# Kernel tuning notes

Hardware: AMD Instinct MI355X
Metric: run time of the kernel (lower is better)

Reference implementation:

```python
import jax, jax.numpy as jnp
import numpy as np

B, S, E, A, DK, H = 8, 2048, 256, 16, 64, 64  # batch, seq, embed, action, d_key, mlp hidden


def setup_inputs() -> dict:
    key = jax.random.key(0)
    ks = jax.random.split(key, 8)
    obs = jax.random.normal(ks[0], (B, S, E), dtype=jnp.float32)
    act = jnp.zeros((B, S, A), dtype=jnp.float32)  # one-hot actions; unused by forward
    # projection weights stored as [in, out] (torch Linear applies x @ W.T)
    Wq = jax.random.normal(ks[1], (E, DK), dtype=jnp.float32) / np.sqrt(E)
    Wk = jax.random.normal(ks[2], (E, DK), dtype=jnp.float32) / np.sqrt(E)
    Wv = jax.random.normal(ks[3], (E, DK), dtype=jnp.float32) / np.sqrt(E)
    W1 = jax.random.normal(ks[4], (DK, H), dtype=jnp.float32) / np.sqrt(DK)
    b1 = jnp.zeros((H,), dtype=jnp.float32)
    W2 = jax.random.normal(ks[5], (H, 1), dtype=jnp.float32) / np.sqrt(H)
    b2 = jnp.zeros((1,), dtype=jnp.float32)
    return dict(obs=obs, act=act, Wq=Wq, Wk=Wk, Wv=Wv, W1=W1, b1=b1, W2=W2, b2=b2)


def reference(obs, act, Wq, Wk, Wv, W1, b1, W2, b2):
    b, s, _ = obs.shape
    dk = Wq.shape[1]
    scale = dk ** -0.25  # applied to both q and k, net 1/sqrt(dk)
    q = (obs @ Wq) * scale          # [b, s, dk]
    k = (obs @ Wk) * scale          # [b, s, dk]
    v = obs @ Wv                    # [b, s, dk]
    scores = jnp.einsum('bqd,bkd->bqk', q, k)  # [b, s, s]
    causal = jnp.tril(jnp.ones((s, s), dtype=bool))
    scores = jnp.where(causal[None], scores, -jnp.inf)
    attn = jax.nn.softmax(scores, axis=2)      # [b, s, s]
    attn_out = jnp.einsum('bqk,bkd->bqd', attn, v)  # [b, s, dk]
    h = jax.nn.relu(attn_out.reshape(b * s, dk) @ W1 + b1)
    x = h @ W2 + b2                 # [b*s, 1]
    return (x, attn)
```

## Files before the change

### kernel.cpp

```cpp
#include <hip/hip_runtime.h>
#include <hip/hip_bf16.h>
#include <math.h>

#define NB 8
#define SQ 2048
#define EMB 256

typedef __attribute__((ext_vector_type(8))) short short8;
typedef __attribute__((ext_vector_type(4))) float f32x4;

__device__ __forceinline__ short f2bf(float f) {
    union { float f; unsigned u; } v; v.f = f;
    unsigned r = v.u + 0x7FFF + ((v.u >> 16) & 1);
    return (short)(r >> 16);
}

__global__ __launch_bounds__(256) void k_wt(const float* __restrict__ Wq,
                                            const float* __restrict__ Wk,
                                            const float* __restrict__ Wv,
                                            short* __restrict__ wt) {
    int o = blockIdx.x * 256 + threadIdx.x;
    int row = o >> 8, e = o & 255;
    int w = row >> 6, d = row & 63;
    const float* W = (w == 0) ? Wq : ((w == 1) ? Wk : Wv);
    wt[o] = f2bf(W[e * 64 + d]);
}

__global__ __launch_bounds__(256) void k_proj(const float* __restrict__ obs,
                                              const short* __restrict__ wt,
                                              short* __restrict__ qw,
                                              short* __restrict__ kw,
                                              short* __restrict__ vt) {
    int tid = threadIdx.x, w = tid >> 6, l = tid & 63;
    int rb = blockIdx.x;
    int r0 = rb * 64 + w * 16;
    int arow = r0 + (l & 15);
    int eo = (l >> 4) * 8;
    f32x4 acc[12];
    #pragma unroll
    for (int c = 0; c < 12; ++c) acc[c] = (f32x4){0.f, 0.f, 0.f, 0.f};
    #pragma unroll
    for (int ks = 0; ks < 8; ++ks) {
        int e0 = ks * 32;
        const float* ap = obs + (size_t)arow * 256 + e0 + eo;
        float4 f0 = *(const float4*)ap;
        float4 f1 = *(const float4*)(ap + 4);
        short8 a;
        a[0] = f2bf(f0.x); a[1] = f2bf(f0.y); a[2] = f2bf(f0.z); a[3] = f2bf(f0.w);
        a[4] = f2bf(f1.x); a[5] = f2bf(f1.y); a[6] = f2bf(f1.z); a[7] = f2bf(f1.w);
        #pragma unroll
        for (int c = 0; c < 12; ++c) {
            short8 bf = *(const short8*)(wt + (size_t)(c * 16 + (l & 15)) * 256 + e0 + eo);
            acc[c] = __builtin_amdgcn_mfma_f32_16x16x32_bf16(a, bf, acc[c], 0, 0, 0);
        }
    }
    const float scale = 0.35355339059327373f;
    __shared__ short ldsv[64][72];
    int rloc = w * 16 + (l >> 4) * 4;
    int col16 = l & 15;
    #pragma unroll
    for (int c = 0; c < 12; ++c) {
        #pragma unroll
        for (int r = 0; r < 4; ++r) {
            float val = acc[c][r];
            int row = r0 + (l >> 4) * 4 + r;
            if (c < 4) {
                qw[(size_t)row * 64 + c * 16 + col16] = f2bf(val * scale);
            } else if (c < 8) {
                kw[(size_t)row * 64 + (c - 4) * 16 + col16] = f2bf(val * scale);
            } else {
                ldsv[(c - 8) * 16 + col16][rloc + r] = f2bf(val);
            }
        }
    }
    __syncthreads();
    int b = (rb * 64) >> 11;
    int s0 = (rb * 64) & 2047;
    int d = tid >> 2, ch = (tid & 3) * 16;
    short* dst = vt + (size_t)b * 64 * 2048 + (size_t)d * 2048 + s0 + ch;
    #pragma unroll
    for (int j = 0; j < 16; ++j) dst[j] = ldsv[d][ch + j];
}

__global__ __launch_bounds__(256) void k_flash(const short* __restrict__ qw,
                                               const short* __restrict__ kw,
                                               const short* __restrict__ vt,
                                               float* __restrict__ ao,
                                               float* __restrict__ ml) {
    int qb = blockIdx.x, b = blockIdx.y;
    int q0 = qb * 64;
    int tid = threadIdx.x, w = tid >> 6, l = tid & 63;
    int lg = l >> 4, lc = l & 15;
    int r0 = q0 + w * 16;
    int eo = lg * 8;
    __shared__ short ldsP[4][16][72];
    const short* qbase = qw + (size_t)b * SQ * 64;
    const short* kbase = kw + (size_t)b * SQ * 64;
    const short* vbase = vt + (size_t)b * 64 * SQ;
    short8 qf0 = *(const short8*)(qbase + (size_t)(r0 + lc) * 64 + eo);
    short8 qf1 = *(const short8*)(qbase + (size_t)(r0 + lc) * 64 + 32 + eo);
    float m[4], lsum[4];
    f32x4 o[4];
    #pragma unroll
    for (int r = 0; r < 4; ++r) { m[r] = -INFINITY; lsum[r] = 0.f; }
    #pragma unroll
    for (int nj = 0; nj < 4; ++nj) o[nj] = (f32x4){0.f, 0.f, 0.f, 0.f};

    for (int kb = 0; kb <= qb; ++kb) {
        int k0 = kb * 64;
        f32x4 s[4];
        #pragma unroll
        for (int nj = 0; nj < 4; ++nj) s[nj] = (f32x4){0.f, 0.f, 0.f, 0.f};
        #pragma unroll
        for (int nj = 0; nj < 4; ++nj) {
            short8 kf = *(const short8*)(kbase + (size_t)(k0 + nj * 16 + lc) * 64 + eo);
            s[nj] = __builtin_amdgcn_mfma_f32_16x16x32_bf16(qf0, kf, s[nj], 0, 0, 0);
        }
        #pragma unroll
        for (int nj = 0; nj < 4; ++nj) {
            short8 kf = *(const short8*)(kbase + (size_t)(k0 + nj * 16 + lc) * 64 + 32 + eo);
            s[nj] = __builtin_amdgcn_mfma_f32_16x16x32_bf16(qf1, kf, s[nj], 0, 0, 0);
        }
        if (kb == qb) {
            #pragma unroll
            for (int nj = 0; nj < 4; ++nj)
                #pragma unroll
                for (int r = 0; r < 4; ++r)
                    if (k0 + nj * 16 + lc > r0 + lg * 4 + r) s[nj][r] = -INFINITY;
        }
        #pragma unroll
        for (int r = 0; r < 4; ++r) {
            float pm = fmaxf(fmaxf(s[0][r], s[1][r]), fmaxf(s[2][r], s[3][r]));
            pm = fmaxf(pm, __shfl_xor(pm, 1));
            pm = fmaxf(pm, __shfl_xor(pm, 2));
            pm = fmaxf(pm, __shfl_xor(pm, 4));
            pm = fmaxf(pm, __shfl_xor(pm, 8));
            float mn = fmaxf(m[r], pm);
            float sc = __expf(m[r] - mn);
            m[r] = mn;
            lsum[r] *= sc;
            #pragma unroll
            for (int nj = 0; nj < 4; ++nj) o[nj][r] *= sc;
            float ps = 0.f;
            #pragma unroll
            for (int nj = 0; nj < 4; ++nj) {
                float p = __expf(s[nj][r] - mn);
                ps += p;
                ldsP[w][lg * 4 + r][nj * 16 + lc] = f2bf(p);
            }
            ps += __shfl_xor(ps, 1);
            ps += __shfl_xor(ps, 2);
            ps += __shfl_xor(ps, 4);
            ps += __shfl_xor(ps, 8);
            lsum[r] += ps;
        }
        #pragma unroll
        for (int ks = 0; ks < 2; ++ks) {
            short8 pa = *(const short8*)&ldsP[w][lc][ks * 32 + lg * 8];
            #pragma unroll
            for (int nj = 0; nj < 4; ++nj) {
                short8 vf = *(const short8*)(vbase + (size_t)(nj * 16 + lc) * SQ + k0 + ks * 32 + eo);
                o[nj] = __builtin_amdgcn_mfma_f32_16x16x32_bf16(pa, vf, o[nj], 0, 0, 0);
            }
        }
    }
    #pragma unroll
    for (int r = 0; r < 4; ++r) {
        float inv = 1.f / lsum[r];
        int row = r0 + lg * 4 + r;
        if (lc == 0) {
            ml[((size_t)b * SQ + row) * 2]     = m[r];
            ml[((size_t)b * SQ + row) * 2 + 1] = inv;
        }
        #pragma unroll
        for (int nj = 0; nj < 4; ++nj)
            ao[((size_t)b * SQ + row) * 64 + nj * 16 + lc] = o[nj][r] * inv;
    }
}

__global__ __launch_bounds__(256) void k_attnw(const short* __restrict__ qw,
                                               const short* __restrict__ kw,
                                               const float* __restrict__ ml,
                                               float* __restrict__ attn) {
    int kb = blockIdx.x, qb = blockIdx.y, b = blockIdx.z;
    int q0 = qb * 64, k0 = kb * 64;
    float* abase = attn + (size_t)b * SQ * SQ;
    int tid = threadIdx.x;
    if (kb > qb) {
        int row = q0 + (tid >> 2);
        float4* dst = (float4*)(abase + (size_t)row * SQ + k0 + (tid & 3) * 16);
        float4 z = {0.f, 0.f, 0.f, 0.f};
        dst[0] = z; dst[1] = z; dst[2] = z; dst[3] = z;
        return;
    }
    int w = tid >> 6, l = tid & 63, lg = l >> 4, lc = l & 15;
    int r0 = q0 + w * 16, eo = lg * 8;
    const short* qbase = qw + (size_t)b * SQ * 64;
    const short* kbase = kw + (size_t)b * SQ * 64;
    short8 qf0 = *(const short8*)(qbase + (size_t)(r0 + lc) * 64 + eo);
    short8 qf1 = *(const short8*)(qbase + (size_t)(r0 + lc) * 64 + 32 + eo);
    f32x4 s[4];
    #pragma unroll
    for (int nj = 0; nj < 4; ++nj) s[nj] = (f32x4){0.f, 0.f, 0.f, 0.f};
    #pragma unroll
    for (int nj = 0; nj < 4; ++nj) {
        short8 kf = *(const short8*)(kbase + (size_t)(k0 + nj * 16 + lc) * 64 + eo);
        s[nj] = __builtin_amdgcn_mfma_f32_16x16x32_bf16(qf0, kf, s[nj], 0, 0, 0);
    }
    #pragma unroll
    for (int nj = 0; nj < 4; ++nj) {
        short8 kf = *(const short8*)(kbase + (size_t)(k0 + nj * 16 + lc) * 64 + 32 + eo);
        s[nj] = __builtin_amdgcn_mfma_f32_16x16x32_bf16(qf1, kf, s[nj], 0, 0, 0);
    }
    #pragma unroll
    for (int r = 0; r < 4; ++r) {
        int row = r0 + lg * 4 + r;
        float mr = ml[((size_t)b * SQ + row) * 2];
        float iv = ml[((size_t)b * SQ + row) * 2 + 1];
        #pragma unroll
        for (int nj = 0; nj < 4; ++nj) {
            int col = k0 + nj * 16 + lc;
            float p = (col <= row) ? __expf(s[nj][r] - mr) * iv : 0.f;
            abase[(size_t)row * SQ + col] = p;
        }
    }
}

__global__ __launch_bounds__(256) void k_mlp(const float* __restrict__ ao,
                                             const float* __restrict__ W1,
                                             const float* __restrict__ b1,
                                             const float* __restrict__ W2,
                                             const float* __restrict__ b2,
                                             float* __restrict__ x) {
    int tid = threadIdx.x, w = tid >> 6, l = tid & 63;
    int grow = blockIdx.x * 4 + w;
    __shared__ float lds[4][64];
    lds[w][l] = ao[(size_t)grow * 64 + l];
    __syncthreads();
    float acc = b1[l];
    #pragma unroll
    for (int d = 0; d < 64; ++d) acc += lds[w][d] * W1[d * 64 + l];
    float h = fmaxf(acc, 0.f);
    float p = h * W2[l];
    #pragma unroll
    for (int o = 32; o > 0; o >>= 1) p += __shfl_xor(p, o);
    if (l == 0) x[grow] = p + b2[0];
}

extern "C" void kernel_launch(void* const* d_in, const int* in_sizes, int n_in,
                              void* d_out, int out_size, void* d_ws, size_t ws_size,
                              hipStream_t stream) {
    const float* obs = (const float*)d_in[0];
    const float* Wq  = (const float*)d_in[2];
    const float* Wk  = (const float*)d_in[3];
    const float* Wv  = (const float*)d_in[4];
    const float* W1  = (const float*)d_in[5];
    const float* b1  = (const float*)d_in[6];
    const float* W2  = (const float*)d_in[7];
    const float* b2  = (const float*)d_in[8];

    float* x    = (float*)d_out;
    float* attn = (float*)d_out + NB * SQ;

    char* ws = (char*)d_ws;
    short* wt = (short*)(ws);
    short* qw = (short*)(ws + 131072);
    short* kw = (short*)(ws + 2228224);
    short* vt = (short*)(ws + 4325376);
    float* ml = (float*)(ws + 6422528);
    float* ao = (float*)(ws + 6553600);

    k_wt<<<dim3(192), dim3(256), 0, stream>>>(Wq, Wk, Wv, wt);
    k_proj<<<dim3(256), dim3(256), 0, stream>>>(obs, wt, qw, kw, vt);
    k_flash<<<dim3(32, NB), dim3(256), 0, stream>>>(qw, kw, vt, ao, ml);
    k_attnw<<<dim3(32, 32, NB), dim3(256), 0, stream>>>(qw, kw, ml, attn);
    k_mlp<<<dim3(4096), dim3(256), 0, stream>>>(ao, W1, b1, W2, b2, x);
}
```

Measured before the change: 152.4 us.

## Fuse flash attention, attention-weight write and MLP into one split-K kernel

Merges the flash-attention, attention-matrix and MLP kernels into a single kernel. Each 512-thread block handles 32 query rows and splits the key blocks across 8 waves, then merges the partial softmax states through LDS atomics. Blocks are scheduled heaviest-first, and the intermediate attention output and max/sum buffers no longer make a round trip through global memory. The projection kernel is also re-tiled to 16 rows per block for more parallelism. The cost is that QK^T is computed twice within one kernel, plus extra LDS reduction and barriers.

```diff
diff --git a/kernel.cpp b/kernel.cpp
--- a/kernel.cpp
+++ b/kernel.cpp
@@ -4,7 +4,8 @@
 
 #define NB 8
 #define SQ 2048
-#define EMB 256
+#define QR 32
+#define NW 8
 
 typedef __attribute__((ext_vector_type(8))) short short8;
 typedef __attribute__((ext_vector_type(4))) float f32x4;
@@ -26,225 +27,250 @@
     wt[o] = f2bf(W[e * 64 + d]);
 }
 
-__global__ __launch_bounds__(256) void k_proj(const float* __restrict__ obs,
-                                              const short* __restrict__ wt,
-                                              short* __restrict__ qw,
-                                              short* __restrict__ kw,
-                                              short* __restrict__ vt) {
-    int tid = threadIdx.x, w = tid >> 6, l = tid & 63;
-    int rb = blockIdx.x;
-    int r0 = rb * 64 + w * 16;
-    int arow = r0 + (l & 15);
-    int eo = (l >> 4) * 8;
-    f32x4 acc[12];
-    #pragma unroll
-    for (int c = 0; c < 12; ++c) acc[c] = (f32x4){0.f, 0.f, 0.f, 0.f};
+__global__ __launch_bounds__(256, 4) void k_proj(const float* __restrict__ obs,
+                                                 const short* __restrict__ wt,
+                                                 short* __restrict__ qw,
+                                                 short* __restrict__ kw,
+                                                 short* __restrict__ vt) {
+    int tid = threadIdx.x, w = tid >> 6, l = tid & 63, lg = l >> 4, lc = l & 15;
+    int r0 = blockIdx.x * 16;
+    int arow = r0 + lc;
+    f32x4 accq = {0.f,0.f,0.f,0.f}, acck = {0.f,0.f,0.f,0.f}, accv = {0.f,0.f,0.f,0.f};
+    const short* wq = wt + (size_t)(w * 16 + lc) * 256;
+    const short* wk = wt + (size_t)(64 + w * 16 + lc) * 256;
+    const short* wv = wt + (size_t)(128 + w * 16 + lc) * 256;
     #pragma unroll
     for (int ks = 0; ks < 8; ++ks) {
-        int e0 = ks * 32;
-        const float* ap = obs + (size_t)arow * 256 + e0 + eo;
+        int e0 = ks * 32 + lg * 8;
+        const float* ap = obs + (size_t)arow * 256 + e0;
         float4 f0 = *(const float4*)ap;
         float4 f1 = *(const float4*)(ap + 4);
         short8 a;
         a[0] = f2bf(f0.x); a[1] = f2bf(f0.y); a[2] = f2bf(f0.z); a[3] = f2bf(f0.w);
         a[4] = f2bf(f1.x); a[5] = f2bf(f1.y); a[6] = f2bf(f1.z); a[7] = f2bf(f1.w);
-        #pragma unroll
-        for (int c = 0; c < 12; ++c) {
-            short8 bf = *(const short8*)(wt + (size_t)(c * 16 + (l & 15)) * 256 + e0 + eo);
-            acc[c] = __builtin_amdgcn_mfma_f32_16x16x32_bf16(a, bf, acc[c], 0, 0, 0);
-        }
+        accq = __builtin_amdgcn_mfma_f32_16x16x32_bf16(a, *(const short8*)(wq + e0), accq, 0, 0, 0);
+        acck = __builtin_amdgcn_mfma_f32_16x16x32_bf16(a, *(const short8*)(wk + e0), acck, 0, 0, 0);
+        accv = __builtin_amdgcn_mfma_f32_16x16x32_bf16(a, *(const short8*)(wv + e0), accv, 0, 0, 0);
     }
     const float scale = 0.35355339059327373f;
-    __shared__ short ldsv[64][72];
-    int rloc = w * 16 + (l >> 4) * 4;
-    int col16 = l & 15;
-    #pragma unroll
-    for (int c = 0; c < 12; ++c) {
-        #pragma unroll
-        for (int r = 0; r < 4; ++r) {
-            float val = acc[c][r];
-            int row = r0 + (l >> 4) * 4 + r;
-            if (c < 4) {
-                qw[(size_t)row * 64 + c * 16 + col16] = f2bf(val * scale);
-            } else if (c < 8) {
-                kw[(size_t)row * 64 + (c - 4) * 16 + col16] = f2bf(val * scale);
-            } else {
-                ldsv[(c - 8) * 16 + col16][rloc + r] = f2bf(val);
-            }
-        }
+    __shared__ short ldsv[64][18];
+    #pragma unroll
+    for (int r = 0; r < 4; ++r) {
+        int row = r0 + lg * 4 + r;
+        qw[(size_t)row * 64 + w * 16 + lc] = f2bf(accq[r] * scale);
+        kw[(size_t)row * 64 + w * 16 + lc] = f2bf(acck[r] * scale);
+        ldsv[w * 16 + lc][lg * 4 + r] = f2bf(accv[r]);
     }
     __syncthreads();
-    int b = (rb * 64) >> 11;
-    int s0 = (rb * 64) & 2047;
-    int d = tid >> 2, ch = (tid & 3) * 16;
-    short* dst = vt + (size_t)b * 64 * 2048 + (size_t)d * 2048 + s0 + ch;
-    #pragma unroll
-    for (int j = 0; j < 16; ++j) dst[j] = ldsv[d][ch + j];
-}
-
-__global__ __launch_bounds__(256) void k_flash(const short* __restrict__ qw,
-                                               const short* __restrict__ kw,
-                                               const short* __restrict__ vt,
-                                               float* __restrict__ ao,
-                                               float* __restrict__ ml) {
-    int qb = blockIdx.x, b = blockIdx.y;
-    int q0 = qb * 64;
-    int tid = threadIdx.x, w = tid >> 6, l = tid & 63;
-    int lg = l >> 4, lc = l & 15;
-    int r0 = q0 + w * 16;
-    int eo = lg * 8;
-    __shared__ short ldsP[4][16][72];
+    int b = r0 >> 11, s0 = r0 & 2047;
+    int d = tid >> 2, sc = (tid & 3) * 4;
+    short* dst = vt + (size_t)b * 64 * SQ + (size_t)d * SQ + s0 + sc;
+    dst[0] = ldsv[d][sc]; dst[1] = ldsv[d][sc + 1];
+    dst[2] = ldsv[d][sc + 2]; dst[3] = ldsv[d][sc + 3];
+}
+
+__global__ __launch_bounds__(512, 2) void k_fused(const short* __restrict__ qw,
+                                                  const short* __restrict__ kw,
+                                                  const short* __restrict__ vt,
+                                                  const float* __restrict__ W1,
+                                                  const float* __restrict__ b1,
+                                                  const float* __restrict__ W2,
+                                                  const float* __restrict__ b2,
+                                                  float* __restrict__ x,
+                                                  float* __restrict__ attn) {
+    int bx = blockIdx.x;
+    int sq = 63 - (bx >> 3);
+    int b  = bx & 7;
+    int s0 = sq * QR;
+    int tid = threadIdx.x, w = tid >> 6, l = tid & 63, lg = l >> 4, lc = l & 15;
+    int kbmax = sq >> 1;
+
+    __shared__ short ldsP[NW][QR][72];
+    __shared__ float o_acc[QR][72];
+    __shared__ float mw[NW][QR], lw[NW][QR];
+    __shared__ float mfin[QR], linv[QR];
+
     const short* qbase = qw + (size_t)b * SQ * 64;
     const short* kbase = kw + (size_t)b * SQ * 64;
     const short* vbase = vt + (size_t)b * 64 * SQ;
-    short8 qf0 = *(const short8*)(qbase + (size_t)(r0 + lc) * 64 + eo);
-    short8 qf1 = *(const short8*)(qbase + (size_t)(r0 + lc) * 64 + 32 + eo);
-    float m[4], lsum[4];
-    f32x4 o[4];
-    #pragma unroll
-    for (int r = 0; r < 4; ++r) { m[r] = -INFINITY; lsum[r] = 0.f; }
-    #pragma unroll
-    for (int nj = 0; nj < 4; ++nj) o[nj] = (f32x4){0.f, 0.f, 0.f, 0.f};
-
-    for (int kb = 0; kb <= qb; ++kb) {
+
+    short8 qf[2][2];
+    #pragma unroll
+    for (int mi = 0; mi < 2; ++mi)
+        #pragma unroll
+        for (int ks = 0; ks < 2; ++ks)
+            qf[mi][ks] = *(const short8*)(qbase + (size_t)(s0 + mi * 16 + lc) * 64 + ks * 32 + lg * 8);
+
+    f32x4 o[2][4];
+    float m[8], ls[8];
+    #pragma unroll
+    for (int i = 0; i < 8; ++i) { m[i] = -INFINITY; ls[i] = 0.f; }
+    #pragma unroll
+    for (int mi = 0; mi < 2; ++mi)
+        #pragma unroll
+        for (int nj = 0; nj < 4; ++nj) o[mi][nj] = (f32x4){0.f,0.f,0.f,0.f};
+
+    for (int kb = w; kb <= kbmax; kb += NW) {
         int k0 = kb * 64;
-        f32x4 s[4];
-        #pragma unroll
-        for (int nj = 0; nj < 4; ++nj) s[nj] = (f32x4){0.f, 0.f, 0.f, 0.f};
+        f32x4 s[2][4];
+        #pragma unroll
+        for (int mi = 0; mi < 2; ++mi)
+            #pragma unroll
+            for (int nj = 0; nj < 4; ++nj) s[mi][nj] = (f32x4){0.f,0.f,0.f,0.f};
         #pragma unroll
         for (int nj = 0; nj < 4; ++nj) {
-            short8 kf = *(const short8*)(kbase + (size_t)(k0 + nj * 16 + lc) * 64 + eo);
-            s[nj] = __builtin_amdgcn_mfma_f32_16x16x32_bf16(qf0, kf, s[nj], 0, 0, 0);
-        }
+            short8 kf0 = *(const short8*)(kbase + (size_t)(k0 + nj * 16 + lc) * 64 + lg * 8);
+            short8 kf1 = *(const short8*)(kbase + (size_t)(k0 + nj * 16 + lc) * 64 + 32 + lg * 8);
+            #pragma unroll
+            for (int mi = 0; mi < 2; ++mi) {
+                s[mi][nj] = __builtin_amdgcn_mfma_f32_16x16x32_bf16(qf[mi][0], kf0, s[mi][nj], 0, 0, 0);
+                s[mi][nj] = __builtin_amdgcn_mfma_f32_16x16x32_bf16(qf[mi][1], kf1, s[mi][nj], 0, 0, 0);
+            }
+        }
+        if (kb == kbmax) {
+            #pragma unroll
+            for (int mi = 0; mi < 2; ++mi)
+                #pragma unroll
+                for (int nj = 0; nj < 4; ++nj)
+                    #pragma unroll
+                    for (int r = 0; r < 4; ++r)
+                        if (k0 + nj * 16 + lc > s0 + mi * 16 + lg * 4 + r) s[mi][nj][r] = -INFINITY;
+        }
+        #pragma unroll
+        for (int mi = 0; mi < 2; ++mi)
+            #pragma unroll
+            for (int r = 0; r < 4; ++r) {
+                int ri = mi * 4 + r;
+                int rowloc = mi * 16 + lg * 4 + r;
+                float pm = fmaxf(fmaxf(s[mi][0][r], s[mi][1][r]), fmaxf(s[mi][2][r], s[mi][3][r]));
+                pm = fmaxf(pm, __shfl_xor(pm, 1));
+                pm = fmaxf(pm, __shfl_xor(pm, 2));
+                pm = fmaxf(pm, __shfl_xor(pm, 4));
+                pm = fmaxf(pm, __shfl_xor(pm, 8));
+                float mn = fmaxf(m[ri], pm);
+                float sc = __expf(m[ri] - mn);
+                m[ri] = mn;
+                ls[ri] *= sc;
+                #pragma unroll
+                for (int nj = 0; nj < 4; ++nj) o[mi][nj][r] *= sc;
+                float ps = 0.f;
+                #pragma unroll
+                for (int nj = 0; nj < 4; ++nj) {
+                    float p = __expf(s[mi][nj][r] - mn);
+                    ps += p;
+                    ldsP[w][rowloc][nj * 16 + lc] = f2bf(p);
+                }
+                ps += __shfl_xor(ps, 1);
+                ps += __shfl_xor(ps, 2);
+                ps += __shfl_xor(ps, 4);
+                ps += __shfl_xor(ps, 8);
+                ls[ri] += ps;
+            }
+        #pragma unroll
+        for (int ks = 0; ks < 2; ++ks) {
+            short8 pa0 = *(const short8*)&ldsP[w][lc][ks * 32 + lg * 8];
+            short8 pa1 = *(const short8*)&ldsP[w][16 + lc][ks * 32 + lg * 8];
+            #pragma unroll
+            for (int nj = 0; nj < 4; ++nj) {
+                short8 vf = *(const short8*)(vbase + (size_t)(nj * 16 + lc) * SQ + k0 + ks * 32 + lg * 8);
+                o[0][nj] = __builtin_amdgcn_mfma_f32_16x16x32_bf16(pa0, vf, o[0][nj], 0, 0, 0);
+                o[1][nj] = __builtin_amdgcn_mfma_f32_16x16x32_bf16(pa1, vf, o[1][nj], 0, 0, 0);
+            }
+        }
+    }
+
+    #pragma unroll
+    for (int mi = 0; mi < 2; ++mi)
+        #pragma unroll
+        for (int r = 0; r < 4; ++r) {
+            int rowloc = mi * 16 + lg * 4 + r;
+            if (lc == 0) { mw[w][rowloc] = m[mi * 4 + r]; lw[w][rowloc] = ls[mi * 4 + r]; }
+        }
+    for (int idx = tid; idx < QR * 72; idx += 512) ((float*)o_acc)[idx] = 0.f;
+    __syncthreads();
+    #pragma unroll
+    for (int mi = 0; mi < 2; ++mi)
+        #pragma unroll
+        for (int r = 0; r < 4; ++r) {
+            int rowloc = mi * 16 + lg * 4 + r;
+            float mf = mw[0][rowloc];
+            #pragma unroll
+            for (int ww = 1; ww < NW; ++ww) mf = fmaxf(mf, mw[ww][rowloc]);
+            float f = __expf(m[mi * 4 + r] - mf);
+            #pragma unroll
+            for (int nj = 0; nj < 4; ++nj)
+                atomicAdd(&o_acc[rowloc][nj * 16 + lc], o[mi][nj][r] * f);
+        }
+    __syncthreads();
+
+    #pragma unroll
+    for (int rr = 0; rr < 4; ++rr) {
+        int rowloc = w * 4 + rr;
+        float mf = mw[0][rowloc];
+        #pragma unroll
+        for (int ww = 1; ww < NW; ++ww) mf = fmaxf(mf, mw[ww][rowloc]);
+        float lf = 0.f;
+        #pragma unroll
+        for (int ww = 0; ww < NW; ++ww) lf += __expf(mw[ww][rowloc] - mf) * lw[ww][rowloc];
+        float inv = 1.f / lf;
+        if (l == 0) { mfin[rowloc] = mf; linv[rowloc] = inv; }
+        float t = 0.f;
+        #pragma unroll 8
+        for (int d = 0; d < 64; ++d) t += o_acc[rowloc][d] * W1[d * 64 + l];
+        float h = fmaxf(t * inv + b1[l], 0.f);
+        float px = h * W2[l];
+        px += __shfl_xor(px, 1);
+        px += __shfl_xor(px, 2);
+        px += __shfl_xor(px, 4);
+        px += __shfl_xor(px, 8);
+        px += __shfl_xor(px, 16);
+        px += __shfl_xor(px, 32);
+        if (l == 0) x[(size_t)b * SQ + s0 + rowloc] = px + b2[0];
+    }
+    __syncthreads();
+
+    float* abase = attn + (size_t)b * SQ * SQ;
+    for (int kb = w; kb < 32; kb += NW) {
+        int k0 = kb * 64;
+        if (kb > kbmax) {
+            float4 z = {0.f,0.f,0.f,0.f};
+            #pragma unroll
+            for (int rep = 0; rep < 8; ++rep) {
+                int row = s0 + rep * 4 + lg;
+                *(float4*)(abase + (size_t)row * SQ + k0 + lc * 4) = z;
+            }
+            continue;
+        }
+        f32x4 s[2][4];
+        #pragma unroll
+        for (int mi = 0; mi < 2; ++mi)
+            #pragma unroll
+            for (int nj = 0; nj < 4; ++nj) s[mi][nj] = (f32x4){0.f,0.f,0.f,0.f};
         #pragma unroll
         for (int nj = 0; nj < 4; ++nj) {
-            short8 kf = *(const short8*)(kbase + (size_t)(k0 + nj * 16 + lc) * 64 + 32 + eo);
-            s[nj] = __builtin_amdgcn_mfma_f32_16x16x32_bf16(qf1, kf, s[nj], 0, 0, 0);
-        }
-        if (kb == qb) {
-            #pragma unroll
-            for (int nj = 0; nj < 4; ++nj)
+            short8 kf0 = *(const short8*)(kbase + (size_t)(k0 + nj * 16 + lc) * 64 + lg * 8);
+            short8 kf1 = *(const short8*)(kbase + (size_t)(k0 + nj * 16 + lc) * 64 + 32 + lg * 8);
+            #pragma unroll
+            for (int mi = 0; mi < 2; ++mi) {
+                s[mi][nj] = __builtin_amdgcn_mfma_f32_16x16x32_bf16(qf[mi][0], kf0, s[mi][nj], 0, 0, 0);
+                s[mi][nj] = __builtin_amdgcn_mfma_f32_16x16x32_bf16(qf[mi][1], kf1, s[mi][nj], 0, 0, 0);
+            }
+        }
+        #pragma unroll
+        for (int mi = 0; mi < 2; ++mi)
+            #pragma unroll
+            for (int r = 0; r < 4; ++r) {
+                int rowloc = mi * 16 + lg * 4 + r;
+                int row = s0 + rowloc;
+                float mf = mfin[rowloc], iv = linv[rowloc];
                 #pragma unroll
-                for (int r = 0; r < 4; ++r)
-                    if (k0 + nj * 16 + lc > r0 + lg * 4 + r) s[nj][r] = -INFINITY;
-        }
-        #pragma unroll
-        for (int r = 0; r < 4; ++r) {
-            float pm = fmaxf(fmaxf(s[0][r], s[1][r]), fmaxf(s[2][r], s[3][r]));
-            pm = fmaxf(pm, __shfl_xor(pm, 1));
-            pm = fmaxf(pm, __shfl_xor(pm, 2));
-            pm = fmaxf(pm, __shfl_xor(pm, 4));
-            pm = fmaxf(pm, __shfl_xor(pm, 8));
-            float mn = fmaxf(m[r], pm);
-            float sc = __expf(m[r] - mn);
-            m[r] = mn;
-            lsum[r] *= sc;
-            #pragma unroll
-            for (int nj = 0; nj < 4; ++nj) o[nj][r] *= sc;
-            float ps = 0.f;
-            #pragma unroll
-            for (int nj = 0; nj < 4; ++nj) {
-                float p = __expf(s[nj][r] - mn);
-                ps += p;
-                ldsP[w][lg * 4 + r][nj * 16 + lc] = f2bf(p);
-            }
-            ps += __shfl_xor(ps, 1);
-            ps += __shfl_xor(ps, 2);
-            ps += __shfl_xor(ps, 4);
-            ps += __shfl_xor(ps, 8);
-            lsum[r] += ps;
-        }
-        #pragma unroll
-        for (int ks = 0; ks < 2; ++ks) {
-            short8 pa = *(const short8*)&ldsP[w][lc][ks * 32 + lg * 8];
-            #pragma unroll
-            for (int nj = 0; nj < 4; ++nj) {
-                short8 vf = *(const short8*)(vbase + (size_t)(nj * 16 + lc) * SQ + k0 + ks * 32 + eo);
-                o[nj] = __builtin_amdgcn_mfma_f32_16x16x32_bf16(pa, vf, o[nj], 0, 0, 0);
-            }
-        }
-    }
-    #pragma unroll
-    for (int r = 0; r < 4; ++r) {
-        float inv = 1.f / lsum[r];
-        int row = r0 + lg * 4 + r;
-        if (lc == 0) {
-            ml[((size_t)b * SQ + row) * 2]     = m[r];
-            ml[((size_t)b * SQ + row) * 2 + 1] = inv;
-        }
-        #pragma unroll
-        for (int nj = 0; nj < 4; ++nj)
-            ao[((size_t)b * SQ + row) * 64 + nj * 16 + lc] = o[nj][r] * inv;
-    }
-}
-
-__global__ __launch_bounds__(256) void k_attnw(const short* __restrict__ qw,
-                                               const short* __restrict__ kw,
-                                               const float* __restrict__ ml,
-                                               float* __restrict__ attn) {
-    int kb = blockIdx.x, qb = blockIdx.y, b = blockIdx.z;
-    int q0 = qb * 64, k0 = kb * 64;
-    float* abase = attn + (size_t)b * SQ * SQ;
-    int tid = threadIdx.x;
-    if (kb > qb) {
-        int row = q0 + (tid >> 2);
-        float4* dst = (float4*)(abase + (size_t)row * SQ + k0 + (tid & 3) * 16);
-        float4 z = {0.f, 0.f, 0.f, 0.f};
-        dst[0] = z; dst[1] = z; dst[2] = z; dst[3] = z;
-        return;
-    }
-    int w = tid >> 6, l = tid & 63, lg = l >> 4, lc = l & 15;
-    int r0 = q0 + w * 16, eo = lg * 8;
-    const short* qbase = qw + (size_t)b * SQ * 64;
-    const short* kbase = kw + (size_t)b * SQ * 64;
-    short8 qf0 = *(const short8*)(qbase + (size_t)(r0 + lc) * 64 + eo);
-    short8 qf1 = *(const short8*)(qbase + (size_t)(r0 + lc) * 64 + 32 + eo);
-    f32x4 s[4];
-    #pragma unroll
-    for (int nj = 0; nj < 4; ++nj) s[nj] = (f32x4){0.f, 0.f, 0.f, 0.f};
-    #pragma unroll
-    for (int nj = 0; nj < 4; ++nj) {
-        short8 kf = *(const short8*)(kbase + (size_t)(k0 + nj * 16 + lc) * 64 + eo);
-        s[nj] = __builtin_amdgcn_mfma_f32_16x16x32_bf16(qf0, kf, s[nj], 0, 0, 0);
-    }
-    #pragma unroll
-    for (int nj = 0; nj < 4; ++nj) {
-        short8 kf = *(const short8*)(kbase + (size_t)(k0 + nj * 16 + lc) * 64 + 32 + eo);
-        s[nj] = __builtin_amdgcn_mfma_f32_16x16x32_bf16(qf1, kf, s[nj], 0, 0, 0);
-    }
-    #pragma unroll
-    for (int r = 0; r < 4; ++r) {
-        int row = r0 + lg * 4 + r;
-        float mr = ml[((size_t)b * SQ + row) * 2];
-        float iv = ml[((size_t)b * SQ + row) * 2 + 1];
-        #pragma unroll
-        for (int nj = 0; nj < 4; ++nj) {
-            int col = k0 + nj * 16 + lc;
-            float p = (col <= row) ? __expf(s[nj][r] - mr) * iv : 0.f;
-            abase[(size_t)row * SQ + col] = p;
-        }
-    }
-}
-
-__global__ __launch_bounds__(256) void k_mlp(const float* __restrict__ ao,
-                                             const float* __restrict__ W1,
-                                             const float* __restrict__ b1,
-                                             const float* __restrict__ W2,
-                                             const float* __restrict__ b2,
-                                             float* __restrict__ x) {
-    int tid = threadIdx.x, w = tid >> 6, l = tid & 63;
-    int grow = blockIdx.x * 4 + w;
-    __shared__ float lds[4][64];
-    lds[w][l] = ao[(size_t)grow * 64 + l];
-    __syncthreads();
-    float acc = b1[l];
-    #pragma unroll
-    for (int d = 0; d < 64; ++d) acc += lds[w][d] * W1[d * 64 + l];
-    float h = fmaxf(acc, 0.f);
-    float p = h * W2[l];
-    #pragma unroll
-    for (int o = 32; o > 0; o >>= 1) p += __shfl_xor(p, o);
-    if (l == 0) x[grow] = p + b2[0];
+                for (int nj = 0; nj < 4; ++nj) {
+                    int col = k0 + nj * 16 + lc;
+                    float p = (col <= row) ? __expf(s[mi][nj][r] - mf) * iv : 0.f;
+                    abase[(size_t)row * SQ + col] = p;
+                }
+            }
+    }
 }
 
 extern "C" void kernel_launch(void* const* d_in, const int* in_sizes, int n_in,
@@ -267,12 +293,8 @@
     short* qw = (short*)(ws + 131072);
     short* kw = (short*)(ws + 2228224);
     short* vt = (short*)(ws + 4325376);
-    float* ml = (float*)(ws + 6422528);
-    float* ao = (float*)(ws + 6553600);
 
     k_wt<<<dim3(192), dim3(256), 0, stream>>>(Wq, Wk, Wv, wt);
-    k_proj<<<dim3(256), dim3(256), 0, stream>>>(obs, wt, qw, kw, vt);
-    k_flash<<<dim3(32, NB), dim3(256), 0, stream>>>(qw, kw, vt, ao, ml);
-    k_attnw<<<dim3(32, 32, NB), dim3(256), 0, stream>>>(qw, kw, ml, attn);
-    k_mlp<<<dim3(4096), dim3(256), 0, stream>>>(ao, W1, b1, W2, b2, x);
-}
+    k_proj<<<dim3(1024), dim3(256), 0, stream>>>(obs, wt, qw, kw, vt);
+    k_fused<<<dim3(512), dim3(512), 0, stream>>>(qw, kw, vt, W1, b1, W2, b2, x, attn);
+}
```

New measurement: 136.9 us. 10.2% less time.

## Split flash attention across key blocks and fuse combine with MLP

Applied to the files above, without the earlier changes.

The flash kernel now splits each query block's key loop across eight strided partitions, which raises the block count from 256 to up to 2048. It writes unnormalized partial outputs and (m, l) pairs into the attn output buffer, which serves as scratch until k_attnw overwrites it. A new combine kernel merges the partitions with log-sum-exp weights, writes the final m and 1/l, and runs the MLP in the same kernel, so the separate MLP launch and the ao round trip are gone. The projection kernel is also regridded to 16 rows per block with 4x more blocks. The combine step adds extra global traffic for the partials, and its scalar MLP loop runs with fewer blocks.

```diff
diff --git a/kernel.cpp b/kernel.cpp
--- a/kernel.cpp
+++ b/kernel.cpp
@@ -4,7 +4,7 @@
 
 #define NB 8
 #define SQ 2048
-#define EMB 256
+#define NSP 8
 
 typedef __attribute__((ext_vector_type(8))) short short8;
 typedef __attribute__((ext_vector_type(4))) float f32x4;
@@ -26,71 +26,57 @@
     wt[o] = f2bf(W[e * 64 + d]);
 }
 
-__global__ __launch_bounds__(256) void k_proj(const float* __restrict__ obs,
-                                              const short* __restrict__ wt,
-                                              short* __restrict__ qw,
-                                              short* __restrict__ kw,
-                                              short* __restrict__ vt) {
-    int tid = threadIdx.x, w = tid >> 6, l = tid & 63;
-    int rb = blockIdx.x;
-    int r0 = rb * 64 + w * 16;
-    int arow = r0 + (l & 15);
-    int eo = (l >> 4) * 8;
-    f32x4 acc[12];
-    #pragma unroll
-    for (int c = 0; c < 12; ++c) acc[c] = (f32x4){0.f, 0.f, 0.f, 0.f};
+__global__ __launch_bounds__(256, 4) void k_proj(const float* __restrict__ obs,
+                                                 const short* __restrict__ wt,
+                                                 short* __restrict__ qw,
+                                                 short* __restrict__ kw,
+                                                 short* __restrict__ vt) {
+    int tid = threadIdx.x, w = tid >> 6, l = tid & 63, lg = l >> 4, lc = l & 15;
+    int r0 = blockIdx.x * 16;
+    int arow = r0 + lc;
+    f32x4 accq = {0.f,0.f,0.f,0.f}, acck = {0.f,0.f,0.f,0.f}, accv = {0.f,0.f,0.f,0.f};
+    const short* wq = wt + (size_t)(w * 16 + lc) * 256;
+    const short* wk = wt + (size_t)(64 + w * 16 + lc) * 256;
+    const short* wv = wt + (size_t)(128 + w * 16 + lc) * 256;
     #pragma unroll
     for (int ks = 0; ks < 8; ++ks) {
-        int e0 = ks * 32;
-        const float* ap = obs + (size_t)arow * 256 + e0 + eo;
+        int e0 = ks * 32 + lg * 8;
+        const float* ap = obs + (size_t)arow * 256 + e0;
         float4 f0 = *(const float4*)ap;
         float4 f1 = *(const float4*)(ap + 4);
         short8 a;
         a[0] = f2bf(f0.x); a[1] = f2bf(f0.y); a[2] = f2bf(f0.z); a[3] = f2bf(f0.w);
         a[4] = f2bf(f1.x); a[5] = f2bf(f1.y); a[6] = f2bf(f1.z); a[7] = f2bf(f1.w);
-        #pragma unroll
-        for (int c = 0; c < 12; ++c) {
-            short8 bf = *(const short8*)(wt + (size_t)(c * 16 + (l & 15)) * 256 + e0 + eo);
-            acc[c] = __builtin_amdgcn_mfma_f32_16x16x32_bf16(a, bf, acc[c], 0, 0, 0);
-        }
+        accq = __builtin_amdgcn_mfma_f32_16x16x32_bf16(a, *(const short8*)(wq + e0), accq, 0, 0, 0);
+        acck = __builtin_amdgcn_mfma_f32_16x16x32_bf16(a, *(const short8*)(wk + e0), acck, 0, 0, 0);
+        accv = __builtin_amdgcn_mfma_f32_16x16x32_bf16(a, *(const short8*)(wv + e0), accv, 0, 0, 0);
     }
     const float scale = 0.35355339059327373f;
-    __shared__ short ldsv[64][72];
-    int rloc = w * 16 + (l >> 4) * 4;
-    int col16 = l & 15;
-    #pragma unroll
-    for (int c = 0; c < 12; ++c) {
-        #pragma unroll
-        for (int r = 0; r < 4; ++r) {
-            float val = acc[c][r];
-            int row = r0 + (l >> 4) * 4 + r;
-            if (c < 4) {
-                qw[(size_t)row * 64 + c * 16 + col16] = f2bf(val * scale);
-            } else if (c < 8) {
-                kw[(size_t)row * 64 + (c - 4) * 16 + col16] = f2bf(val * scale);
-            } else {
-                ldsv[(c - 8) * 16 + col16][rloc + r] = f2bf(val);
-            }
-        }
+    __shared__ short ldsv[64][18];
+    #pragma unroll
+    for (int r = 0; r < 4; ++r) {
+        int row = r0 + lg * 4 + r;
+        qw[(size_t)row * 64 + w * 16 + lc] = f2bf(accq[r] * scale);
+        kw[(size_t)row * 64 + w * 16 + lc] = f2bf(acck[r] * scale);
+        ldsv[w * 16 + lc][lg * 4 + r] = f2bf(accv[r]);
     }
     __syncthreads();
-    int b = (rb * 64) >> 11;
-    int s0 = (rb * 64) & 2047;
-    int d = tid >> 2, ch = (tid & 3) * 16;
-    short* dst = vt + (size_t)b * 64 * 2048 + (size_t)d * 2048 + s0 + ch;
-    #pragma unroll
-    for (int j = 0; j < 16; ++j) dst[j] = ldsv[d][ch + j];
+    int b = r0 >> 11, s0 = r0 & 2047;
+    int d = tid >> 2, sc = (tid & 3) * 4;
+    short* dst = vt + (size_t)b * 64 * SQ + (size_t)d * SQ + s0 + sc;
+    dst[0] = ldsv[d][sc]; dst[1] = ldsv[d][sc + 1];
+    dst[2] = ldsv[d][sc + 2]; dst[3] = ldsv[d][sc + 3];
 }
 
 __global__ __launch_bounds__(256) void k_flash(const short* __restrict__ qw,
                                                const short* __restrict__ kw,
                                                const short* __restrict__ vt,
-                                               float* __restrict__ ao,
-                                               float* __restrict__ ml) {
-    int qb = blockIdx.x, b = blockIdx.y;
+                                               float* __restrict__ op,
+                                               float* __restrict__ mlpart) {
+    int qb = blockIdx.x, sp = blockIdx.y, b = blockIdx.z;
+    if (sp > qb) return;
     int q0 = qb * 64;
-    int tid = threadIdx.x, w = tid >> 6, l = tid & 63;
-    int lg = l >> 4, lc = l & 15;
+    int tid = threadIdx.x, w = tid >> 6, l = tid & 63, lg = l >> 4, lc = l & 15;
     int r0 = q0 + w * 16;
     int eo = lg * 8;
     __shared__ short ldsP[4][16][72];
@@ -106,7 +92,7 @@
     #pragma unroll
     for (int nj = 0; nj < 4; ++nj) o[nj] = (f32x4){0.f, 0.f, 0.f, 0.f};
 
-    for (int kb = 0; kb <= qb; ++kb) {
+    for (int kb = sp; kb <= qb; kb += NSP) {
         int k0 = kb * 64;
         f32x4 s[4];
         #pragma unroll
@@ -164,23 +150,100 @@
             }
         }
     }
+    size_t pb = ((size_t)sp * NB + b) * SQ;
     #pragma unroll
     for (int r = 0; r < 4; ++r) {
-        float inv = 1.f / lsum[r];
         int row = r0 + lg * 4 + r;
         if (lc == 0) {
-            ml[((size_t)b * SQ + row) * 2]     = m[r];
-            ml[((size_t)b * SQ + row) * 2 + 1] = inv;
+            mlpart[(pb + row) * 2]     = m[r];
+            mlpart[(pb + row) * 2 + 1] = lsum[r];
         }
         #pragma unroll
         for (int nj = 0; nj < 4; ++nj)
-            ao[((size_t)b * SQ + row) * 64 + nj * 16 + lc] = o[nj][r] * inv;
+            op[(pb + row) * 64 + nj * 16 + lc] = o[nj][r];
+    }
+}
+
+__global__ __launch_bounds__(256) void k_combine(const float* __restrict__ op,
+                                                 const float* __restrict__ mlpart,
+                                                 const float* __restrict__ W1,
+                                                 const float* __restrict__ b1,
+                                                 const float* __restrict__ W2,
+                                                 const float* __restrict__ b2,
+                                                 float* __restrict__ x,
+                                                 float* __restrict__ mlf) {
+    int qb = blockIdx.x, b = blockIdx.y;
+    int s0 = qb * 64;
+    int nsp = (qb + 1 < NSP) ? (qb + 1) : NSP;
+    int tid = threadIdx.x;
+    __shared__ float wgt[NSP][64];
+    __shared__ float linv_s[64];
+    __shared__ float ao[64][68];
+    if (tid < 64) {
+        int row = s0 + tid;
+        float mm[NSP], ll[NSP];
+        float mf = -INFINITY;
+        #pragma unroll
+        for (int sp = 0; sp < NSP; ++sp) {
+            if (sp < nsp) {
+                mm[sp] = mlpart[(((size_t)sp * NB + b) * SQ + row) * 2];
+                ll[sp] = mlpart[(((size_t)sp * NB + b) * SQ + row) * 2 + 1];
+            } else { mm[sp] = -INFINITY; ll[sp] = 0.f; }
+            mf = fmaxf(mf, mm[sp]);
+        }
+        float lf = 0.f;
+        #pragma unroll
+        for (int sp = 0; sp < NSP; ++sp) {
+            float wv = __expf(mm[sp] - mf);
+            wgt[sp][tid] = wv;
+            lf += wv * ll[sp];
+        }
+        float inv = 1.f / lf;
+        linv_s[tid] = inv;
+        mlf[((size_t)b * SQ + row) * 2]     = mf;
+        mlf[((size_t)b * SQ + row) * 2 + 1] = inv;
+    }
+    __syncthreads();
+    int row = tid >> 2, cg = (tid & 3) * 16;
+    float acc[16];
+    #pragma unroll
+    for (int j = 0; j < 16; ++j) acc[j] = 0.f;
+    for (int sp = 0; sp < NSP; ++sp) {
+        if (sp >= nsp) break;
+        const float* src = op + (((size_t)sp * NB + b) * SQ + s0 + row) * 64 + cg;
+        float wv = wgt[sp][row];
+        #pragma unroll
+        for (int j = 0; j < 4; ++j) {
+            float4 v = *(const float4*)(src + j * 4);
+            acc[j*4+0] += wv * v.x; acc[j*4+1] += wv * v.y;
+            acc[j*4+2] += wv * v.z; acc[j*4+3] += wv * v.w;
+        }
+    }
+    float inv = linv_s[row];
+    #pragma unroll
+    for (int j = 0; j < 16; ++j) ao[row][cg + j] = acc[j] * inv;
+    __syncthreads();
+    int w = tid >> 6, l = tid & 63;
+    for (int rr = 0; rr < 16; ++rr) {
+        int rowloc = w * 16 + rr;
+        float t = 0.f;
+        #pragma unroll 8
+        for (int d = 0; d < 64; ++d) t += ao[rowloc][d] * W1[d * 64 + l];
+        float h = fmaxf(t + b1[l], 0.f);
+        float px = h * W2[l];
+        px += __shfl_xor(px, 1);
+        px += __shfl_xor(px, 2);
+        px += __shfl_xor(px, 4);
+        px += __shfl_xor(px, 8);
+        px += __shfl_xor(px, 16);
+        px += __shfl_xor(px, 32);
+        if (l == 0) x[(size_t)b * SQ + s0 + rowloc] = px + b2[0];
     }
 }
 
 __global__ __launch_bounds__(256) void k_attnw(const short* __restrict__ qw,
                                                const short* __restrict__ kw,
-                                               const float* __restrict__ ml,
+                                               const float* __restrict__ mlf,
                                                float* __restrict__ attn) {
     int kb = blockIdx.x, qb = blockIdx.y, b = blockIdx.z;
     int q0 = qb * 64, k0 = kb * 64;
@@ -215,8 +278,8 @@
     #pragma unroll
     for (int r = 0; r < 4; ++r) {
         int row = r0 + lg * 4 + r;
-        float mr = ml[((size_t)b * SQ + row) * 2];
-        float iv = ml[((size_t)b * SQ + row) * 2 + 1];
+        float mr = mlf[((size_t)b * SQ + row) * 2];
+        float iv = mlf[((size_t)b * SQ + row) * 2 + 1];
         #pragma unroll
         for (int nj = 0; nj < 4; ++nj) {
             int col = k0 + nj * 16 + lc;
@@ -224,27 +287,6 @@
             abase[(size_t)row * SQ + col] = p;
         }
     }
-}
-
-__global__ __launch_bounds__(256) void k_mlp(const float* __restrict__ ao,
-                                             const float* __restrict__ W1,
-                                             const float* __restrict__ b1,
-                                             const float* __restrict__ W2,
-                                             const float* __restrict__ b2,
-                                             float* __restrict__ x) {
-    int tid = threadIdx.x, w = tid >> 6, l = tid & 63;
-    int grow = blockIdx.x * 4 + w;
-    __shared__ float lds[4][64];
-    lds[w][l] = ao[(size_t)grow * 64 + l];
-    __syncthreads();
-    float acc = b1[l];
-    #pragma unroll
-    for (int d = 0; d < 64; ++d) acc += lds[w][d] * W1[d * 64 + l];
-    float h = fmaxf(acc, 0.f);
-    float p = h * W2[l];
-    #pragma unroll
-    for (int o = 32; o > 0; o >>= 1) p += __shfl_xor(p, o);
-    if (l == 0) x[grow] = p + b2[0];
 }
 
 extern "C" void kernel_launch(void* const* d_in, const int* in_sizes, int n_in,
@@ -262,17 +304,19 @@
     float* x    = (float*)d_out;
     float* attn = (float*)d_out + NB * SQ;
 
+    float* op     = attn;
+    float* mlpart = attn + (size_t)NSP * NB * SQ * 64;
+
     char* ws = (char*)d_ws;
-    short* wt = (short*)(ws);
-    short* qw = (short*)(ws + 131072);
-    short* kw = (short*)(ws + 2228224);
-    short* vt = (short*)(ws + 4325376);
-    float* ml = (float*)(ws + 6422528);
-    float* ao = (float*)(ws + 6553600);
+    short* wt  = (short*)(ws);
+    short* qw  = (short*)(ws + 131072);
+    short* kw  = (short*)(ws + 2228224);
+    short* vt  = (short*)(ws + 4325376);
+    float* mlf = (float*)(ws + 6422528);
 
     k_wt<<<dim3(192), dim3(256), 0, stream>>>(Wq, Wk, Wv, wt);
-    k_proj<<<dim3(256), dim3(256), 0, stream>>>(obs, wt, qw, kw, vt);
-    k_flash<<<dim3(32, NB), dim3(256), 0, stream>>>(qw, kw, vt, ao, ml);
-    k_attnw<<<dim3(32, 32, NB), dim3(256), 0, stream>>>(qw, kw, ml, attn);
-    k_mlp<<<dim3(4096), dim3(256), 0, stream>>>(ao, W1, b1, W2, b2, x);
-}
+    k_proj<<<dim3(1024), dim3(256), 0, stream>>>(obs, wt, qw, kw, vt);
+    k_flash<<<dim3(32, NSP, NB), dim3(256), 0, stream>>>(qw, kw, vt, op, mlpart);
+    k_combine<<<dim3(32, NB), dim3(256), 0, stream>>>(op, mlpart, W1, b1, W2, b2, x, mlf);
+    k_attnw<<<dim3(32, 32, NB), dim3(256), 0, stream>>>(qw, kw, mlf, attn);
+}
```

Result: slower. 170.2 us (+11.7%).
